# Performance work log

Hardware: AMD Instinct MI355X
Metric: run time of the kernel (lower is better)

Reference implementation:

```python
import jax, jax.numpy as jnp
import numpy as np

D_MODEL = 512
NUM_HEADS = 8
HEAD_DIM = D_MODEL // NUM_HEADS
LN_EPS = 1e-5


def setup_inputs() -> dict:
    key = jax.random.key(0)
    ks = jax.random.split(key, 12)
    B, S, D = 4, 8192, D_MODEL
    scale = 1.0 / np.sqrt(D)  # xavier-ish init
    inp = {
        "x": jax.random.normal(ks[0], (B, S, D), dtype=jnp.float32),
        "Wq": jax.random.normal(ks[1], (D, D), dtype=jnp.float32) * scale,
        "bq": jnp.zeros((D,), dtype=jnp.float32),
        "Wk": jax.random.normal(ks[2], (D, D), dtype=jnp.float32) * scale,
        "bk": jnp.zeros((D,), dtype=jnp.float32),
        "Wv": jax.random.normal(ks[3], (D, D), dtype=jnp.float32) * scale,
        "bv": jnp.zeros((D,), dtype=jnp.float32),
        "Wo": jax.random.normal(ks[4], (D, D), dtype=jnp.float32) * scale,
        "bo": jnp.zeros((D,), dtype=jnp.float32),
        "gamma": jnp.ones((D,), dtype=jnp.float32),
        "beta": jnp.zeros((D,), dtype=jnp.float32),
    }
    return inp


def _split_heads(t, B, S):
    # (B, S, D) -> (B, H, S, hd)
    return t.reshape(B, S, NUM_HEADS, HEAD_DIM).transpose(0, 2, 1, 3)


def _feature_map(t):
    return jax.nn.elu(t) + 1.0


def reference(x, Wq, bq, Wk, bk, Wv, bv, Wo, bo, gamma, beta):
    B, S, D = x.shape
    q = _split_heads(x @ Wq + bq, B, S)
    k = _split_heads(x @ Wk + bk, B, S)
    v = _split_heads(x @ Wv + bv, B, S)

    q = _feature_map(q)
    k = _feature_map(k)

    # kv summary: (B, H, hd, hd) -- O(n d^2) instead of O(n^2 d)
    kv = jnp.einsum('bhnd,bhnm->bhdm', k, v)
    out = jnp.einsum('bhnd,bhdm->bhnm', q, kv)

    k_sum = k.sum(axis=2)  # (B, H, hd)
    normalizer = jnp.clip(jnp.einsum('bhnd,bhd->bhn', q, k_sum), 1e-6, None)
    out = out / normalizer[..., None]

    # merge heads: (B, H, S, hd) -> (B, S, D)
    out = out.transpose(0, 2, 1, 3).reshape(B, S, D)
    out = out @ Wo + bo

    # residual + layer norm (dropout is identity in eval / p=0)
    y = x + out
    mean = y.mean(axis=-1, keepdims=True)
    var = y.var(axis=-1, keepdims=True)
    y = (y - mean) * jax.lax.rsqrt(var + LN_EPS)
    return y * gamma + beta
```

## Files before the change

kernel.cpp:

```cpp
#include <hip/hip_runtime.h>
#include <cstdint>

#define SEQ     8192
#define BATCH   4
#define NHEAD   8
#define NTOK    (BATCH*SEQ)

typedef __bf16 bf16x8 __attribute__((ext_vector_type(8)));
typedef float  floatx4 __attribute__((ext_vector_type(4)));

static __device__ __forceinline__ uint16_t f2b(float f) {
    uint32_t u = __float_as_uint(f);
    u += 0x7fffu + ((u >> 16) & 1u);
    return (uint16_t)(u >> 16);
}

static __device__ __forceinline__ void async_copy16(const uint16_t* g, uint16_t* l) {
#if __has_builtin(__builtin_amdgcn_global_load_lds)
    __builtin_amdgcn_global_load_lds(
        (const __attribute__((address_space(1))) void*)g,
        (__attribute__((address_space(3))) void*)l, 16, 0, 0);
#else
    *(uint4*)l = *(const uint4*)g;
#endif
}

__global__ __launch_bounds__(256) void convert_x(
    const float* __restrict__ X, uint16_t* __restrict__ Xb)
{
    const size_t i = ((size_t)blockIdx.x * 256 + threadIdx.x) * 8;
    float4 f0 = *(const float4*)(X + i);
    float4 f1 = *(const float4*)(X + i + 4);
    uint4 o;
    uint16_t* p = (uint16_t*)&o;
    p[0]=f2b(f0.x); p[1]=f2b(f0.y); p[2]=f2b(f0.z); p[3]=f2b(f0.w);
    p[4]=f2b(f1.x); p[5]=f2b(f1.y); p[6]=f2b(f1.z); p[7]=f2b(f1.w);
    *(uint4*)(Xb + i) = o;
}

__global__ __launch_bounds__(256) void convert_w(
    const float* __restrict__ Wq, const float* __restrict__ Wk,
    const float* __restrict__ Wv, const float* __restrict__ Wo,
    uint16_t* __restrict__ out)
{
    const int z = blockIdx.z;
    const float* W = (z == 0) ? Wq : (z == 1) ? Wk : (z == 2) ? Wv : Wo;
    uint16_t* o = out + (size_t)z * 262144;
    const int n0 = blockIdx.x * 64, k0 = blockIdx.y * 64;
    __shared__ uint16_t tl[64][64];
    const int t = threadIdx.x;
    const int r  = t >> 4;
    const int c4 = (t & 15) * 4;
    #pragma unroll
    for (int s = 0; s < 4; ++s) {
        const int k = r + s * 16;
        float4 f = *(const float4*)(W + (size_t)(k0 + k) * 512 + n0 + c4);
        tl[c4 + 0][k] = f2b(f.x); tl[c4 + 1][k] = f2b(f.y);
        tl[c4 + 2][k] = f2b(f.z); tl[c4 + 3][k] = f2b(f.w);
    }
    __syncthreads();
    const int n  = t >> 2;
    const int kk = (t & 3) * 16;
    uint4* dst = (uint4*)(o + (size_t)(n0 + n) * 512 + k0 + kk);
    dst[0] = *(const uint4*)&tl[n][kk];
    dst[1] = *(const uint4*)&tl[n][kk + 8];
}

__global__ __launch_bounds__(256) void qkv128(
    const uint16_t* __restrict__ Xb,
    const uint16_t* __restrict__ Wt,
    const float* __restrict__ bq_, const float* __restrict__ bk_,
    const float* __restrict__ bv_,
    uint16_t* __restrict__ outQ, uint16_t* __restrict__ outK,
    uint16_t* __restrict__ outV)
{
    const int id = blockIdx.x;
    const int c  = id & 7;
    const int r_ = id >> 3;
    const int j_ = r_ % 12;
    const int s  = (r_ / 12) * 8 + c;
    const int proj = j_ >> 2;
    const int n0   = (j_ & 3) * 128;
    const int m0   = s * 128;

    const uint16_t* W = Wt + (size_t)proj * 262144;
    const float* bias = (proj == 0) ? bq_ : (proj == 1) ? bk_ : bv_;
    uint16_t* out     = (proj == 0) ? outQ : (proj == 1) ? outK : outV;
    const int act = (proj < 2);

    __shared__ uint16_t smem[128 * 128];
    const int t = threadIdx.x;
    const int wave = t >> 6, lane = t & 63, quad = lane >> 4, lrow = lane & 15;
    const int wm = (wave & 1) * 64, wn = (wave >> 1) * 64;
    const int sr = t >> 2;
    const int sc = (t & 3) * 8;

    floatx4 acc[4][4] = {};

    for (int k0 = 0; k0 < 512; k0 += 64) {
        const uint16_t* gA = Xb + (size_t)(m0 + sr) * 512 + k0 + sc;
        async_copy16(gA,            smem + t * 8);
        async_copy16(gA + 64 * 512, smem + (t + 256) * 8);
        async_copy16(gA + 32,            smem + 4096 + t * 8);
        async_copy16(gA + 64 * 512 + 32, smem + 4096 + (t + 256) * 8);
        const uint16_t* gB = W + (size_t)(n0 + sr) * 512 + k0 + sc;
        async_copy16(gB,            smem + 8192 + t * 8);
        async_copy16(gB + 64 * 512, smem + 8192 + (t + 256) * 8);
        async_copy16(gB + 32,            smem + 12288 + t * 8);
        async_copy16(gB + 64 * 512 + 32, smem + 12288 + (t + 256) * 8);
        __syncthreads();
        #pragma unroll
        for (int h = 0; h < 2; ++h) {
            bf16x8 af[4], bfr[4];
            #pragma unroll
            for (int i = 0; i < 4; ++i)
                af[i] = *(const bf16x8*)(smem + h * 4096 + (wm + i * 16 + lrow) * 32 + quad * 8);
            #pragma unroll
            for (int j = 0; j < 4; ++j)
                bfr[j] = *(const bf16x8*)(smem + 8192 + h * 4096 + (wn + j * 16 + lrow) * 32 + quad * 8);
            #pragma unroll
            for (int i = 0; i < 4; ++i)
                #pragma unroll
                for (int j = 0; j < 4; ++j)
                    acc[i][j] = __builtin_amdgcn_mfma_f32_16x16x32_bf16(af[i], bfr[j], acc[i][j], 0, 0, 0);
        }
        __syncthreads();
    }

    #pragma unroll
    for (int j = 0; j < 4; ++j) {
        const int col = wn + j * 16 + lrow;
        const float bb = bias[n0 + col];
        #pragma unroll
        for (int i = 0; i < 4; ++i) {
            #pragma unroll
            for (int r = 0; r < 4; ++r) {
                const int row = wm + i * 16 + quad * 4 + r;
                float v = acc[i][j][r] + bb;
                if (act) v = (v > 0.0f) ? (v + 1.0f) : __expf(v);
                smem[row * 128 + (col ^ (((row >> 2) & 3) << 4))] = f2b(v);
            }
        }
    }
    __syncthreads();
    #pragma unroll
    for (int p = 0; p < 8; ++p) {
        const int idx = p * 256 + t;
        const int row = idx >> 4;
        const int cc  = (idx & 15) * 8;
        uint4 v = *(const uint4*)(smem + row * 128 + (cc ^ (((row >> 2) & 3) << 4)));
        *(uint4*)(out + (size_t)(m0 + row) * 512 + n0 + cc) = v;
    }
}

__global__ __launch_bounds__(256) void kv_accum(
    const uint16_t* __restrict__ K,
    const uint16_t* __restrict__ V,
    float* __restrict__ KV,
    float* __restrict__ KSUM)
{
    const int chunk = blockIdx.x;
    const int h     = blockIdx.y;
    const int b     = blockIdx.z;
    const int t    = threadIdx.x;
    const int wv   = t >> 6;
    const int lane = t & 63;
    const int quad = lane >> 4;
    const int lrow = lane & 15;

    __shared__ uint16_t kt[64 * 72];
    __shared__ uint16_t vt[64 * 72];

    floatx4 acc[4] = {};
    floatx4 accS = {};
    union { uint16_t u[8]; bf16x8 v; } one_u;
    #pragma unroll
    for (int j = 0; j < 8; ++j) one_u.u[j] = 0x3F80;
    const bf16x8 ones = one_u.v;

    const size_t base = ((size_t)(b * SEQ + chunk * 512)) * 512 + h * 64;

    for (int n0 = 0; n0 < 512; n0 += 64) {
        #pragma unroll
        for (int s = 0; s < 2; ++s) {
            const int i   = t + 256 * s;
            const int tok = i >> 3;
            const int d0  = (i & 7) * 8;
            uint4 kq = *(const uint4*)(K + base + (size_t)(n0 + tok) * 512 + d0);
            const uint16_t* kp = (const uint16_t*)&kq;
            #pragma unroll
            for (int j = 0; j < 8; ++j) kt[(d0 + j) * 72 + tok] = kp[j];
            uint4 vq = *(const uint4*)(V + base + (size_t)(n0 + tok) * 512 + d0);
            const uint16_t* vp = (const uint16_t*)&vq;
            #pragma unroll
            for (int j = 0; j < 8; ++j) vt[(d0 + j) * 72 + tok] = vp[j];
        }
        __syncthreads();
        #pragma unroll
        for (int ks = 0; ks < 2; ++ks) {
            bf16x8 af = *(const bf16x8*)(kt + (wv * 16 + lrow) * 72 + ks * 32 + quad * 8);
            accS = __builtin_amdgcn_mfma_f32_16x16x32_bf16(af, ones, accS, 0, 0, 0);
            #pragma unroll
            for (int nt = 0; nt < 4; ++nt) {
                bf16x8 bf = *(const bf16x8*)(vt + (nt * 16 + lrow) * 72 + ks * 32 + quad * 8);
                acc[nt] = __builtin_amdgcn_mfma_f32_16x16x32_bf16(af, bf, acc[nt], 0, 0, 0);
            }
        }
        __syncthreads();
    }

    float* kvp = KV + (size_t)(b * NHEAD + h) * 4096;
    #pragma unroll
    for (int nt = 0; nt < 4; ++nt) {
        const int m = nt * 16 + lrow;
        #pragma unroll
        for (int r = 0; r < 4; ++r) {
            const int d = wv * 16 + quad * 4 + r;
            atomicAdd(kvp + d * 64 + m, acc[nt][r]);
        }
    }
    if (lrow == 0) {
        float* kp = KSUM + (size_t)(b * NHEAD + h) * 64;
        #pragma unroll
        for (int r = 0; r < 4; ++r)
            atomicAdd(kp + wv * 16 + quad * 4 + r, accS[r]);
    }
}

__global__ __launch_bounds__(256) void attn_apply(
    const uint16_t* __restrict__ Q,
    const float* __restrict__ KVg,
    const float* __restrict__ KSg,
    uint16_t* __restrict__ OUT)
{
    const int h    = blockIdx.y;
    const int tok0 = blockIdx.x * 64;
    const int b    = tok0 >> 13;
    const int t    = threadIdx.x;
    const int wv   = t >> 6;
    const int lane = t & 63;
    const int quad = lane >> 4;
    const int lrow = lane & 15;

    __shared__ uint16_t bt[64 * 72];
    __shared__ uint16_t ksb[64];

    const float* kvp = KVg + (size_t)(b * NHEAD + h) * 4096;
    #pragma unroll
    for (int s = 0; s < 16; ++s) {
        const int e = t + 256 * s;
        const int d = e >> 6, m = e & 63;
        bt[m * 72 + d] = f2b(kvp[e]);
    }
    if (t < 64) ksb[t] = f2b(KSg[(size_t)(b * NHEAD + h) * 64 + t]);
    __syncthreads();

    floatx4 acc[4] = {};
    floatx4 accN = {};
    const uint16_t* qrow = Q + (size_t)(tok0 + wv * 16 + lrow) * 512 + h * 64 + quad * 8;
    #pragma unroll
    for (int ks = 0; ks < 2; ++ks) {
        bf16x8 af = *(const bf16x8*)(qrow + ks * 32);
        bf16x8 bks = *(const bf16x8*)(ksb + ks * 32 + quad * 8);
        accN = __builtin_amdgcn_mfma_f32_16x16x32_bf16(af, bks, accN, 0, 0, 0);
        #pragma unroll
        for (int nt = 0; nt < 4; ++nt) {
            bf16x8 bf = *(const bf16x8*)(bt + (nt * 16 + lrow) * 72 + ks * 32 + quad * 8);
            acc[nt] = __builtin_amdgcn_mfma_f32_16x16x32_bf16(af, bf, acc[nt], 0, 0, 0);
        }
    }

    __syncthreads();
    #pragma unroll
    for (int r = 0; r < 4; ++r) {
        const float inv = 1.0f / fmaxf(accN[r], 1e-6f);
        const int row = wv * 16 + quad * 4 + r;
        #pragma unroll
        for (int nt = 0; nt < 4; ++nt) {
            const int col = nt * 16 + lrow;
            bt[row * 64 + (col ^ (((row >> 2) & 3) << 4))] = f2b(acc[nt][r] * inv);
        }
    }
    __syncthreads();
    #pragma unroll
    for (int p = 0; p < 2; ++p) {
        const int idx = p * 256 + t;
        const int row = idx >> 3;
        const int cc  = (idx & 7) * 8;
        uint4 v = *(const uint4*)(bt + row * 64 + (cc ^ (((row >> 2) & 3) << 4)));
        *(uint4*)(OUT + (size_t)(tok0 + row) * 512 + h * 64 + cc) = v;
    }
}

__global__ __launch_bounds__(256) void gemm_out_ln(
    const uint16_t* __restrict__ A,
    const uint16_t* __restrict__ Wt,
    const float* __restrict__ bias,
    const float* __restrict__ resid,
    const float* __restrict__ gamma,
    const float* __restrict__ beta,
    float* __restrict__ OUT)
{
    const int m0 = blockIdx.x * 64;

    __shared__ uint16_t sA[64 * 32];
    __shared__ uint16_t sB[512 * 32];
    __shared__ float rs[4][64], rs2[4][64];

    const int t = threadIdx.x;
    const int wave = t >> 6, lane = t & 63, quad = lane >> 4, lrow = lane & 15;
    const int wn = wave * 128;
    const int sr = t >> 2;
    const int sc = (t & 3) * 8;

    floatx4 acc[4][8] = {};

    for (int k0 = 0; k0 < 512; k0 += 32) {
        const uint16_t* gA = A + (size_t)(m0 + sr) * 512 + k0 + sc;
        async_copy16(gA, sA + t * 8);
        const uint16_t* gB = Wt + (size_t)sr * 512 + k0 + sc;
        #pragma unroll
        for (int s = 0; s < 8; ++s)
            async_copy16(gB + s * 32768, sB + t * 8 + s * 2048);
        __syncthreads();
        bf16x8 af[4], bfr[8];
        #pragma unroll
        for (int i = 0; i < 4; ++i)
            af[i] = *(const bf16x8*)(sA + (i * 16 + lrow) * 32 + quad * 8);
        #pragma unroll
        for (int j = 0; j < 8; ++j)
            bfr[j] = *(const bf16x8*)(sB + (wn + j * 16 + lrow) * 32 + quad * 8);
        #pragma unroll
        for (int i = 0; i < 4; ++i)
            #pragma unroll
            for (int j = 0; j < 8; ++j)
                acc[i][j] = __builtin_amdgcn_mfma_f32_16x16x32_bf16(af[i], bfr[j], acc[i][j], 0, 0, 0);
        __syncthreads();
    }

    float g[8], be[8], bb[8];
    #pragma unroll
    for (int j = 0; j < 8; ++j) {
        const int col = wn + j * 16 + lrow;
        bb[j] = bias[col];
        g[j]  = gamma[col];
        be[j] = beta[col];
    }
    #pragma unroll
    for (int i = 0; i < 4; ++i) {
        #pragma unroll
        for (int r = 0; r < 4; ++r) {
            const int row = i * 16 + quad * 4 + r;
            const float* rp = resid + (size_t)(m0 + row) * 512 + wn;
            #pragma unroll
            for (int j = 0; j < 8; ++j)
                acc[i][j][r] += bb[j] + rp[j * 16 + lrow];
        }
    }

    #pragma unroll
    for (int i = 0; i < 4; ++i) {
        #pragma unroll
        for (int r = 0; r < 4; ++r) {
            const int row = i * 16 + quad * 4 + r;
            float s = 0.f, s2 = 0.f;
            #pragma unroll
            for (int j = 0; j < 8; ++j) {
                const float v = acc[i][j][r];
                s += v; s2 += v * v;
            }
            #pragma unroll
            for (int off = 8; off > 0; off >>= 1) {
                s  += __shfl_xor(s, off, 64);
                s2 += __shfl_xor(s2, off, 64);
            }
            if (lrow == 0) { rs[wave][row] = s; rs2[wave][row] = s2; }
        }
    }
    __syncthreads();

    #pragma unroll
    for (int i = 0; i < 4; ++i) {
        #pragma unroll
        for (int r = 0; r < 4; ++r) {
            const int row = i * 16 + quad * 4 + r;
            const float tot  = rs[0][row] + rs[1][row] + rs[2][row] + rs[3][row];
            const float tot2 = rs2[0][row] + rs2[1][row] + rs2[2][row] + rs2[3][row];
            const float mean = tot * (1.0f / 512.0f);
            const float var  = tot2 * (1.0f / 512.0f) - mean * mean;
            const float inv  = rsqrtf(var + 1e-5f);
            float* op = OUT + (size_t)(m0 + row) * 512 + wn;
            #pragma unroll
            for (int j = 0; j < 8; ++j)
                op[j * 16 + lrow] = (acc[i][j][r] - mean) * inv * g[j] + be[j];
        }
    }
}

extern "C" void kernel_launch(void* const* d_in, const int* in_sizes, int n_in,
                              void* d_out, int out_size, void* d_ws, size_t ws_size,
                              hipStream_t stream)
{
    (void)in_sizes; (void)n_in; (void)out_size; (void)ws_size;
    const float* x     = (const float*)d_in[0];
    const float* Wq    = (const float*)d_in[1];
    const float* bq    = (const float*)d_in[2];
    const float* Wk    = (const float*)d_in[3];
    const float* bk    = (const float*)d_in[4];
    const float* Wv    = (const float*)d_in[5];
    const float* bv    = (const float*)d_in[6];
    const float* Wo    = (const float*)d_in[7];
    const float* bo    = (const float*)d_in[8];
    const float* gamma = (const float*)d_in[9];
    const float* beta  = (const float*)d_in[10];

    uint8_t* ws = (uint8_t*)d_ws;
    float*    KV   = (float*)ws;
    float*    KSUM = (float*)(ws + (size_t)32 * 4096 * 4);
    uint16_t* Wt   = (uint16_t*)(ws + (size_t)32 * 4096 * 4 + 32 * 64 * 4);
    uint16_t* phiQ = (uint16_t*)(ws + (size_t)32 * 4096 * 4 + 32 * 64 * 4
                                    + (size_t)4 * 262144 * 2);
    uint16_t* Xb   = phiQ + (size_t)NTOK * 512;
    uint16_t* phiK = (uint16_t*)d_out;
    uint16_t* vbuf = (uint16_t*)d_out + (size_t)NTOK * 512;
    uint16_t* attn = Xb;

    hipMemsetAsync(ws, 0, (size_t)32 * 4096 * 4 + 32 * 64 * 4, stream);

    dim3 blk(256);
    convert_x<<<dim3(NTOK * 512 / (256 * 8)), blk, 0, stream>>>(x, Xb);
    convert_w<<<dim3(8, 8, 4), blk, 0, stream>>>(Wq, Wk, Wv, Wo, Wt);
    qkv128<<<dim3(3072), blk, 0, stream>>>(
        Xb, Wt, bq, bk, bv, phiQ, phiK, vbuf);
    kv_accum<<<dim3(16, NHEAD, BATCH), blk, 0, stream>>>(phiK, vbuf, KV, KSUM);
    attn_apply<<<dim3(NTOK / 64, NHEAD), blk, 0, stream>>>(phiQ, KV, KSUM, attn);
    gemm_out_ln<<<dim3(512), blk, 0, stream>>>(
        attn, Wt + (size_t)3 * 262144, bo, x, gamma, beta, (float*)d_out);
}
```

Before: 314.6 us.

## Cut LDS footprint in QKV GEMM and shrink out-proj LN tile rows

Result: slower. 355.8 us (+13.1%).

```diff
diff --git a/kernel.cpp b/kernel.cpp
--- a/kernel.cpp
+++ b/kernel.cpp
@@ -88,7 +88,7 @@
     uint16_t* out     = (proj == 0) ? outQ : (proj == 1) ? outK : outV;
     const int act = (proj < 2);
 
-    __shared__ uint16_t smem[128 * 128];
+    __shared__ uint16_t smem[8192];
     const int t = threadIdx.x;
     const int wave = t >> 6, lane = t & 63, quad = lane >> 4, lrow = lane & 15;
     const int wm = (wave & 1) * 64, wn = (wave >> 1) * 64;
@@ -97,59 +97,58 @@
 
     floatx4 acc[4][4] = {};
 
-    for (int k0 = 0; k0 < 512; k0 += 64) {
+    for (int k0 = 0; k0 < 512; k0 += 32) {
         const uint16_t* gA = Xb + (size_t)(m0 + sr) * 512 + k0 + sc;
         async_copy16(gA,            smem + t * 8);
         async_copy16(gA + 64 * 512, smem + (t + 256) * 8);
-        async_copy16(gA + 32,            smem + 4096 + t * 8);
-        async_copy16(gA + 64 * 512 + 32, smem + 4096 + (t + 256) * 8);
         const uint16_t* gB = W + (size_t)(n0 + sr) * 512 + k0 + sc;
-        async_copy16(gB,            smem + 8192 + t * 8);
-        async_copy16(gB + 64 * 512, smem + 8192 + (t + 256) * 8);
-        async_copy16(gB + 32,            smem + 12288 + t * 8);
-        async_copy16(gB + 64 * 512 + 32, smem + 12288 + (t + 256) * 8);
-        __syncthreads();
-        #pragma unroll
-        for (int h = 0; h < 2; ++h) {
-            bf16x8 af[4], bfr[4];
-            #pragma unroll
-            for (int i = 0; i < 4; ++i)
-                af[i] = *(const bf16x8*)(smem + h * 4096 + (wm + i * 16 + lrow) * 32 + quad * 8);
+        async_copy16(gB,            smem + 4096 + t * 8);
+        async_copy16(gB + 64 * 512, smem + 4096 + (t + 256) * 8);
+        __syncthreads();
+        bf16x8 af[4], bfr[4];
+        #pragma unroll
+        for (int i = 0; i < 4; ++i)
+            af[i] = *(const bf16x8*)(smem + (wm + i * 16 + lrow) * 32 + quad * 8);
+        #pragma unroll
+        for (int j = 0; j < 4; ++j)
+            bfr[j] = *(const bf16x8*)(smem + 4096 + (wn + j * 16 + lrow) * 32 + quad * 8);
+        #pragma unroll
+        for (int i = 0; i < 4; ++i)
             #pragma unroll
             for (int j = 0; j < 4; ++j)
-                bfr[j] = *(const bf16x8*)(smem + 8192 + h * 4096 + (wn + j * 16 + lrow) * 32 + quad * 8);
-            #pragma unroll
-            for (int i = 0; i < 4; ++i)
+                acc[i][j] = __builtin_amdgcn_mfma_f32_16x16x32_bf16(af[i], bfr[j], acc[i][j], 0, 0, 0);
+        __syncthreads();
+    }
+
+    #pragma unroll
+    for (int hh = 0; hh < 2; ++hh) {
+        if ((wave & 1) == hh) {
+            #pragma unroll
+            for (int j = 0; j < 4; ++j) {
+                const int col = wn + j * 16 + lrow;
+                const float bb = bias[n0 + col];
                 #pragma unroll
-                for (int j = 0; j < 4; ++j)
-                    acc[i][j] = __builtin_amdgcn_mfma_f32_16x16x32_bf16(af[i], bfr[j], acc[i][j], 0, 0, 0);
-        }
-        __syncthreads();
-    }
-
-    #pragma unroll
-    for (int j = 0; j < 4; ++j) {
-        const int col = wn + j * 16 + lrow;
-        const float bb = bias[n0 + col];
-        #pragma unroll
-        for (int i = 0; i < 4; ++i) {
-            #pragma unroll
-            for (int r = 0; r < 4; ++r) {
-                const int row = wm + i * 16 + quad * 4 + r;
-                float v = acc[i][j][r] + bb;
-                if (act) v = (v > 0.0f) ? (v + 1.0f) : __expf(v);
-                smem[row * 128 + (col ^ (((row >> 2) & 3) << 4))] = f2b(v);
+                for (int i = 0; i < 4; ++i) {
+                    #pragma unroll
+                    for (int r = 0; r < 4; ++r) {
+                        const int lr = i * 16 + quad * 4 + r;
+                        float v = acc[i][j][r] + bb;
+                        if (act) v = (v > 0.0f) ? (v + 1.0f) : __expf(v);
+                        smem[lr * 128 + (col ^ (((lr >> 2) & 3) << 4))] = f2b(v);
+                    }
+                }
             }
         }
-    }
-    __syncthreads();
-    #pragma unroll
-    for (int p = 0; p < 8; ++p) {
-        const int idx = p * 256 + t;
-        const int row = idx >> 4;
-        const int cc  = (idx & 15) * 8;
-        uint4 v = *(const uint4*)(smem + row * 128 + (cc ^ (((row >> 2) & 3) << 4)));
-        *(uint4*)(out + (size_t)(m0 + row) * 512 + n0 + cc) = v;
+        __syncthreads();
+        #pragma unroll
+        for (int p = 0; p < 4; ++p) {
+            const int idx = p * 256 + t;
+            const int row = idx >> 4;
+            const int cc  = (idx & 15) * 8;
+            uint4 v = *(const uint4*)(smem + row * 128 + (cc ^ (((row >> 2) & 3) << 4)));
+            *(uint4*)(out + (size_t)(m0 + hh * 64 + row) * 512 + n0 + cc) = v;
+        }
+        __syncthreads();
     }
 }
 
@@ -292,7 +291,7 @@
     }
 }
 
-__global__ __launch_bounds__(256) void gemm_out_ln(
+__global__ __launch_bounds__(256, 4) void gemm_out_ln(
     const uint16_t* __restrict__ A,
     const uint16_t* __restrict__ Wt,
     const float* __restrict__ bias,
@@ -301,37 +300,37 @@
     const float* __restrict__ beta,
     float* __restrict__ OUT)
 {
-    const int m0 = blockIdx.x * 64;
-
-    __shared__ uint16_t sA[64 * 32];
+    const int m0 = blockIdx.x * 32;
+
+    __shared__ uint16_t sA[32 * 32];
     __shared__ uint16_t sB[512 * 32];
-    __shared__ float rs[4][64], rs2[4][64];
+    __shared__ float rs[4][32], rs2[4][32];
 
     const int t = threadIdx.x;
     const int wave = t >> 6, lane = t & 63, quad = lane >> 4, lrow = lane & 15;
     const int wn = wave * 128;
-    const int sr = t >> 2;
-    const int sc = (t & 3) * 8;
-
-    floatx4 acc[4][8] = {};
+
+    floatx4 acc[2][8] = {};
 
     for (int k0 = 0; k0 < 512; k0 += 32) {
-        const uint16_t* gA = A + (size_t)(m0 + sr) * 512 + k0 + sc;
-        async_copy16(gA, sA + t * 8);
-        const uint16_t* gB = Wt + (size_t)sr * 512 + k0 + sc;
+        if (t < 128) {
+            uint4 av = *(const uint4*)(A + (size_t)(m0 + (t >> 2)) * 512 + k0 + (t & 3) * 8);
+            *(uint4*)(sA + t * 8) = av;
+        }
+        const uint16_t* gB = Wt + (size_t)(t >> 2) * 512 + k0 + (t & 3) * 8;
         #pragma unroll
         for (int s = 0; s < 8; ++s)
             async_copy16(gB + s * 32768, sB + t * 8 + s * 2048);
         __syncthreads();
-        bf16x8 af[4], bfr[8];
-        #pragma unroll
-        for (int i = 0; i < 4; ++i)
+        bf16x8 af[2], bfr[8];
+        #pragma unroll
+        for (int i = 0; i < 2; ++i)
             af[i] = *(const bf16x8*)(sA + (i * 16 + lrow) * 32 + quad * 8);
         #pragma unroll
         for (int j = 0; j < 8; ++j)
             bfr[j] = *(const bf16x8*)(sB + (wn + j * 16 + lrow) * 32 + quad * 8);
         #pragma unroll
-        for (int i = 0; i < 4; ++i)
+        for (int i = 0; i < 2; ++i)
             #pragma unroll
             for (int j = 0; j < 8; ++j)
                 acc[i][j] = __builtin_amdgcn_mfma_f32_16x16x32_bf16(af[i], bfr[j], acc[i][j], 0, 0, 0);
@@ -347,7 +346,7 @@
         be[j] = beta[col];
     }
     #pragma unroll
-    for (int i = 0; i < 4; ++i) {
+    for (int i = 0; i < 2; ++i) {
         #pragma unroll
         for (int r = 0; r < 4; ++r) {
             const int row = i * 16 + quad * 4 + r;
@@ -359,7 +358,7 @@
     }
 
     #pragma unroll
-    for (int i = 0; i < 4; ++i) {
+    for (int i = 0; i < 2; ++i) {
         #pragma unroll
         for (int r = 0; r < 4; ++r) {
             const int row = i * 16 + quad * 4 + r;
@@ -380,7 +379,7 @@
     __syncthreads();
 
     #pragma unroll
-    for (int i = 0; i < 4; ++i) {
+    for (int i = 0; i < 2; ++i) {
         #pragma unroll
         for (int r = 0; r < 4; ++r) {
             const int row = i * 16 + quad * 4 + r;
@@ -434,6 +433,6 @@
         Xb, Wt, bq, bk, bv, phiQ, phiK, vbuf);
     kv_accum<<<dim3(16, NHEAD, BATCH), blk, 0, stream>>>(phiK, vbuf, KV, KSUM);
     attn_apply<<<dim3(NTOK / 64, NHEAD), blk, 0, stream>>>(phiQ, KV, KSUM, attn);
-    gemm_out_ln<<<dim3(512), blk, 0, stream>>>(
+    gemm_out_ln<<<dim3(1024), blk, 0, stream>>>(
         attn, Wt + (size_t)3 * 262144, bo, x, gamma, beta, (float*)d_out);
 }
```
